# Optimization experiments

Measured on AMD Instinct MI355X. Metric: run time of the kernel, lower is better.

## Reference

```python
import jax, jax.numpy as jnp
import numpy as np

N, E, DIM, NF, ED = 15000, 30000, 64, 3, 1

def _gru_cell(x, h, w_ih, w_hh, b_ih, b_hh):
    gi = x @ w_ih.T + b_ih
    gh = h @ w_hh.T + b_hh
    ir, iz, i_n = jnp.split(gi, 3, axis=-1)
    hr, hz, hn = jnp.split(gh, 3, axis=-1)
    r = jax.nn.sigmoid(ir + hr)
    z = jax.nn.sigmoid(iz + hz)
    n = jnp.tanh(i_n + r * hn)
    return (1.0 - z) * n + z * h

def _lstm_cell(x, h, c, w_ih, w_hh, b_ih, b_hh):
    g = x @ w_ih.T + b_ih + h @ w_hh.T + b_hh
    i, f, gg, o = jnp.split(g, 4, axis=-1)
    c2 = jax.nn.sigmoid(f) * c + jax.nn.sigmoid(i) * jnp.tanh(gg)
    return jax.nn.sigmoid(o) * jnp.tanh(c2), c2

def setup_inputs():
    key = jax.random.key(0)
    ks = jax.random.split(key, 32)
    p = lambda k, shape: jax.random.normal(k, shape, jnp.float32) * 0.05
    return {
        "x": jax.random.normal(ks[0], (N, NF), jnp.float32),
        "edge_index": jax.random.randint(ks[1], (2, E), 0, N),
        "edge_attr": jax.random.uniform(ks[2], (E, ED), jnp.float32),
        "lin0_w": p(ks[3], (DIM, NF)), "lin0_b": p(ks[4], (DIM,)),
        "e1_w": p(ks[5], (DIM, ED)), "e1_b": p(ks[6], (DIM,)),
        "e2_w": p(ks[7], (DIM * DIM, DIM)), "e2_b": p(ks[8], (DIM * DIM,)),
        "root_w": p(ks[9], (DIM, DIM)), "conv_b": p(ks[10], (DIM,)),
        "gru_w_ih": p(ks[11], (3 * DIM, DIM)), "gru_w_hh": p(ks[12], (3 * DIM, DIM)),
        "gru_b_ih": p(ks[13], (3 * DIM,)), "gru_b_hh": p(ks[14], (3 * DIM,)),
        "s2s_w_ih": p(ks[15], (4 * DIM, 2 * DIM)), "s2s_w_hh": p(ks[16], (4 * DIM, DIM)),
        "s2s_b_ih": p(ks[17], (4 * DIM,)), "s2s_b_hh": p(ks[18], (4 * DIM,)),
        "mem_w_ih": p(ks[19], (4 * DIM, 2 * DIM)), "mem_w_hh": p(ks[20], (4 * DIM, DIM)),
        "mem_b_ih": p(ks[21], (4 * DIM,)), "mem_b_hh": p(ks[22], (4 * DIM,)),
        "lin1_w": p(ks[23], (DIM, DIM)), "lin1_b": p(ks[24], (DIM,)),
        "lin3_w": p(ks[25], (1, DIM)), "lin3_b": p(ks[26], (1,)),
    }

def reference(x, edge_index, edge_attr, lin0_w, lin0_b, e1_w, e1_b, e2_w, e2_b,
              root_w, conv_b, gru_w_ih, gru_w_hh, gru_b_ih, gru_b_hh,
              s2s_w_ih, s2s_w_hh, s2s_b_ih, s2s_b_hh,
              mem_w_ih, mem_w_hh, mem_b_ih, mem_b_hh,
              lin1_w, lin1_b, lin3_w, lin3_b):
    n = x.shape[0]
    src, dst = edge_index[0], edge_index[1]
    # per-edge weight matrices from the edge MLP: [E, DIM, DIM] (edge_attr is constant across the 6 conv steps)
    he = jax.nn.relu(edge_attr @ e1_w.T + e1_b)
    We = (he @ e2_w.T + e2_b).reshape(-1, DIM, DIM)
    deg = jax.ops.segment_sum(jnp.ones(src.shape[0], jnp.float32), dst, num_segments=n)
    denom = jnp.maximum(deg, 1.0)[:, None]
    out = jax.nn.relu(x @ lin0_w.T + lin0_b)   # [N, DIM]
    h = out                                    # GRU hidden init = lin0 output
    for _ in range(6):
        msg = jnp.einsum('ei,eio->eo', out[src], We)          # gather + per-edge matmul
        agg = jax.ops.segment_sum(msg, dst, num_segments=n) / denom  # mean aggr
        m = jax.nn.relu(agg + out @ root_w + conv_b)          # NNConv root + bias
        h = _gru_cell(m, h, gru_w_ih, gru_w_hh, gru_b_ih, gru_b_hh)
        out = h
    # Set2Set pooling over a single graph (data.batch is all zeros)
    q_star = jnp.zeros((1, 2 * DIM), x.dtype)
    hs = jnp.zeros((1, DIM), x.dtype)
    cs = jnp.zeros((1, DIM), x.dtype)
    for _ in range(6):
        hs, cs = _lstm_cell(q_star, hs, cs, s2s_w_ih, s2s_w_hh, s2s_b_ih, s2s_b_hh)
        e = out @ hs[0]                     # [N] attention logits
        a = jax.nn.softmax(e)
        r = (a[:, None] * out).sum(0, keepdims=True)  # [1, DIM]
        q_star = jnp.concatenate([hs, r], axis=-1)     # [1, 2*DIM]
    hx, cx = _lstm_cell(q_star, jnp.zeros((1, DIM), x.dtype), jnp.zeros((1, DIM), x.dtype),
                        mem_w_ih, mem_w_hh, mem_b_ih, mem_b_hh)
    o = jax.nn.relu(hx @ lin1_w.T + lin1_b)
    v = o @ lin3_w.T + lin3_b               # [1, 1]
    return v, hx, cx
```

## Files before the change

### kernel.cpp

```cpp
#include <hip/hip_runtime.h>
#include <math.h>

#define Nn 15000
#define NP 15040
#define Ee 30000
#define NB_E 118
#define EB 938

#define OFF_AGG   0
#define OFF_DEG   962560
#define ZERO_END  977560
#define OFF_OUT   977568
#define OFF_DINV  1940128
#define OFF_AT    1955136
#define OFF_BT    2221376
#define OFF_BP    2487616
#define OFF_U     2487680
#define OFF_V     2491840
#define OFF_MC    2496000
#define OFF_PE    2496016
#define OFF_BH    2526016
#define OFF_BC    2533696
#define OFF_SS    2541376
#define OFF_SD    2571376
#define OFF_SA    2601376
#define OFF_SP    2631376
#define OFF_PK    2661376
#define OFF_GMA   2690048
#define OFF_GSA   2690304
#define OFF_GRA   2690560
#define OFF_GMB   2706944
#define OFF_GSB   2707200
#define OFF_GRB   2707456
#define OFF_HS    2723840
#define OFF_CS    2723904
#define OFF_TSA   2723968
#define OFF_TSB   2740352
#define OFF_TMA   2756736
#define OFF_TMB   2773120
#define WS_FLOATS 2789504

__device__ __forceinline__ float sigf(float x) { return 1.0f / (1.0f + expf(-x)); }
__device__ __forceinline__ float bcast(float v, int l) {
    return __int_as_float(__builtin_amdgcn_readlane(__float_as_int(v), l));
}
__device__ __forceinline__ int bcasti(int v, int l) {
    return __builtin_amdgcn_readlane(v, l);
}

__global__ void k_lin0(const float* __restrict__ x, const float* __restrict__ w,
                       const float* __restrict__ b, float* __restrict__ out) {
    int idx = blockIdx.x * 256 + threadIdx.x;
    if (idx >= NP * 64) return;
    int n = idx >> 6, o = idx & 63;
    float v = 0.f;
    if (n < Nn)
        v = fmaxf(b[o] + x[n*3+0]*w[o*3+0] + x[n*3+1]*w[o*3+1] + x[n*3+2]*w[o*3+2], 0.f);
    out[idx] = v;
}

__global__ void k_patterns(const float* __restrict__ e1w, const float* __restrict__ e1b,
                           float* __restrict__ bp, float* __restrict__ u,
                           float* __restrict__ v, int* __restrict__ mc) {
    __shared__ float t[64]; __shared__ int valid[64]; __shared__ float sbp[65]; __shared__ int cnt;
    int k = threadIdx.x;
    float w1 = e1w[k], b1 = e1b[k];
    float tv = 0.f; int va = 0;
    if (w1 != 0.f) { tv = -b1 / w1; va = (tv > 0.f && tv < 1.f) ? 1 : 0; }
    t[k] = tv; valid[k] = va;
    __syncthreads();
    if (va) {
        int rank = 0;
        for (int kk = 0; kk < 64; ++kk)
            if (valid[kk] && (t[kk] < tv || (t[kk] == tv && kk < k))) rank++;
        sbp[rank] = tv;
    }
    if (k == 0) { int c = 0; for (int kk = 0; kk < 64; ++kk) c += valid[kk]; cnt = c; *mc = c; }
    __syncthreads();
    int m = cnt;
    if (k < m) bp[k] = sbp[k];
    for (int j = 0; j <= m; ++j) {
        float lo = (j == 0) ? 0.f : sbp[j-1];
        float hi = (j == m) ? 1.f : sbp[j];
        float c = 0.5f * (lo + hi);
        int msk = (c * w1 + b1) > 0.f;
        u[j*64 + k] = msk ? w1 : 0.f;
        v[j*64 + k] = msk ? b1 : 0.f;
    }
}

__global__ void k_AB2(const float* __restrict__ e2w, const float* __restrict__ e2b,
                      const float* __restrict__ u, const float* __restrict__ v,
                      const int* __restrict__ mc, float* __restrict__ At, float* __restrict__ Bt) {
    int j = blockIdx.x >> 4;
    if (j > *mc) return;
    int qc = blockIdx.x & 15;
    __shared__ float su[64], sv[64];
    if (threadIdx.x < 64) { su[threadIdx.x] = u[j*64+threadIdx.x]; sv[threadIdx.x] = v[j*64+threadIdx.x]; }
    __syncthreads();
    int q = qc*256 + threadIdx.x;
    int i = q >> 6, o = q & 63;
    const float* row = e2w + q*64;
    float a = 0.f, b = 0.f;
    #pragma unroll 8
    for (int k = 0; k < 64; ++k) { float w = row[k]; a = fmaf(su[k], w, a); b = fmaf(sv[k], w, b); }
    At[j*4096 + o*64 + i] = a;
    Bt[j*4096 + o*64 + i] = b + e2b[q];
}

__global__ void k_eprep2(const int* __restrict__ ei, const float* __restrict__ ea,
                         const float* __restrict__ bp, const int* __restrict__ mc,
                         float* __restrict__ deg, int* __restrict__ pe, int* __restrict__ bh) {
    __shared__ int lh[65];
    int tid = threadIdx.x;
    if (tid < 65) lh[tid] = 0;
    __syncthreads();
    int e = blockIdx.x * 256 + tid;
    if (e < Ee) {
        atomicAdd(&deg[ei[Ee + e]], 1.0f);
        float a = ea[e];
        int m = *mc, p = 0;
        for (int j = 0; j < m; ++j) p += (bp[j] <= a) ? 1 : 0;
        pe[e] = p;
        atomicAdd(&lh[p], 1);
    }
    __syncthreads();
    if (tid < 65) bh[blockIdx.x*65 + tid] = lh[tid];
}

__global__ void k_scan2(const float* __restrict__ deg, float* __restrict__ dinv,
                        const int* __restrict__ bh, int* __restrict__ bc) {
    int tid = threadIdx.x;
    if (blockIdx.x < 59) {
        int n = blockIdx.x * 256 + tid;
        if (n < Nn) dinv[n] = 1.0f / fmaxf(deg[n], 1.0f);
        return;
    }
    __shared__ int stot[65]; __shared__ int sbase[65];
    if (tid < 65) {
        int t = 0;
        for (int b = 0; b < NB_E; ++b) t += bh[b*65 + tid];
        stot[tid] = t;
    }
    __syncthreads();
    if (tid == 0) {
        int run = 0;
        for (int j = 0; j < 65; ++j) { sbase[j] = run; run += stot[j]; }
    }
    __syncthreads();
    if (tid < 65) {
        int run = sbase[tid];
        for (int b = 0; b < NB_E; ++b) { bc[b*65 + tid] = run; run += bh[b*65 + tid]; }
    }
}

__global__ void k_scatter2(const int* __restrict__ ei, const float* __restrict__ ea,
                           const int* __restrict__ pe, const int* __restrict__ bc,
                           int* __restrict__ sS, int* __restrict__ sD,
                           float* __restrict__ sA, int* __restrict__ sP) {
    __shared__ int cur[65];
    int tid = threadIdx.x;
    if (tid < 65) cur[tid] = bc[blockIdx.x*65 + tid];
    __syncthreads();
    int e = blockIdx.x * 256 + tid;
    if (e >= Ee) return;
    int p = pe[e];
    int pos = atomicAdd(&cur[p], 1);
    sS[pos] = ei[e]; sD[pos] = ei[Ee + e]; sA[pos] = ea[e]; sP[pos] = p;
}

__global__ void k_wt2(const float* __restrict__ rootw, const float* __restrict__ whh,
                      const float* __restrict__ wih, float* __restrict__ pk) {
    int idx = blockIdx.x * 256 + threadIdx.x;
    if (idx >= 7*4096) return;
    int g = idx >> 12;
    int t = idx & 4095;
    int q4 = t >> 2, k = t & 3;
    int lane = q4 & 63;
    int i4 = q4 >> 6;
    int i = i4*4 + k;
    float v;
    if (g == 0)      v = rootw[i*64 + lane];
    else if (g < 4)  v = whh[((g-1)*64 + lane)*64 + i];
    else             v = wih[((g-4)*64 + lane)*64 + i];
    pk[idx] = v;
}

__global__ void k_wt3(const float* __restrict__ swih, const float* __restrict__ swhh,
                      const float* __restrict__ mwih,
                      float* __restrict__ sa, float* __restrict__ sb,
                      float* __restrict__ ma, float* __restrict__ mb) {
    int idx = blockIdx.x * 256 + threadIdx.x;
    if (idx >= 4*16384) return;
    int t = idx >> 14, r = idx & 16383;
    int i = r >> 8, g = r & 255;
    if (t == 0)      sa[r] = swih[g*128 + i] + swhh[g*64 + i];
    else if (t == 1) sb[r] = swih[g*128 + 64 + i];
    else if (t == 2) ma[r] = mwih[g*128 + i];
    else             mb[r] = mwih[g*128 + 64 + i];
}

__global__ __launch_bounds__(256) void k_edge4(
        const int* __restrict__ sS, const int* __restrict__ sD,
        const float* __restrict__ sA, const int* __restrict__ sP,
        const float* __restrict__ out, const float* __restrict__ At,
        const float* __restrict__ Bt, const float* __restrict__ dinv,
        float* __restrict__ agg) {
    int tid = threadIdx.x, lane = tid & 63;
    int wid = (blockIdx.x * 256 + tid) >> 6;
    const int CH = 8;
    int e0 = wid * CH;
    if (e0 >= Ee) return;
    int e1 = e0 + CH; if (e1 > Ee) e1 = Ee;
    int cnt = e1 - e0;

    int eidx = e0 + lane;
    int msrc = 0, mdst = 0, mp = 0; float ma = 0.f, mdv = 0.f;
    if (lane < cnt) {
        msrc = sS[eidx]; mdst = sD[eidx]; ma = sA[eidx]; mp = sP[eidx];
        mdv = dinv[mdst];
    }

    float Ar[64], Br[64];
    int curp = -1;
    float hv_next = out[bcasti(msrc, 0)*64 + lane];
    for (int j = 0; j < cnt; ++j) {
        float hv = hv_next;
        if (j+1 < cnt) hv_next = out[bcasti(msrc, j+1)*64 + lane];
        int p = bcasti(mp, j);
        if (p != curp) {
            curp = p;
            const float4* Ap4 = (const float4*)(At + p*4096 + lane*64);
            const float4* Bp4 = (const float4*)(Bt + p*4096 + lane*64);
            #pragma unroll
            for (int q = 0; q < 16; ++q) {
                float4 av = Ap4[q], bv = Bp4[q];
                Ar[q*4+0]=av.x; Ar[q*4+1]=av.y; Ar[q*4+2]=av.z; Ar[q*4+3]=av.w;
                Br[q*4+0]=bv.x; Br[q*4+1]=bv.y; Br[q*4+2]=bv.z; Br[q*4+3]=bv.w;
            }
        }
        float a = bcast(ma, j);
        float acc0 = 0.f, acc1 = 0.f;
        #pragma unroll
        for (int i = 0; i < 64; i += 2) {
            float h0 = bcast(hv, i);
            float h1 = bcast(hv, i+1);
            acc0 = fmaf(h0, fmaf(a, Ar[i],   Br[i]),   acc0);
            acc1 = fmaf(h1, fmaf(a, Ar[i+1], Br[i+1]), acc1);
        }
        float acc = (acc0 + acc1) * bcast(mdv, j);
        atomicAdd(&agg[bcasti(mdst, j)*64 + lane], acc);
    }
}

__global__ __launch_bounds__(512, 2) void k_gru9(
        float* __restrict__ out, float* __restrict__ agg,
        const float* __restrict__ pk, const float* __restrict__ convb,
        const float* __restrict__ gbih, const float* __restrict__ gbhh) {
    __shared__ __align__(16) float wL[7*4096];
    int tid = threadIdx.x, lane = tid & 63, w = tid >> 6;
    {
        const float4* src = (const float4*)pk;
        float4* dst = (float4*)wL;
        #pragma unroll
        for (int i = 0; i < 14; ++i) dst[i*512 + tid] = src[i*512 + tid];
    }
    __syncthreads();
    const float4* wL4 = (const float4*)wL;
    int n0 = blockIdx.x*64 + w*8;

    float hv[8], mv[8], ghr[8], ghz[8], ghn[8];
    #pragma unroll
    for (int k = 0; k < 8; ++k) hv[k] = out[(n0+k)*64 + lane];

    float a0[8], a1[8], a2[8], a3[8];
    #pragma unroll
    for (int k = 0; k < 8; ++k) { a0[k]=0.f; a1[k]=0.f; a2[k]=0.f; a3[k]=0.f; }
    #pragma unroll 4
    for (int i4 = 0; i4 < 16; ++i4) {
        float4 w0 = wL4[(0*16+i4)*64 + lane];
        float4 w1 = wL4[(1*16+i4)*64 + lane];
        float4 w2 = wL4[(2*16+i4)*64 + lane];
        float4 w3 = wL4[(3*16+i4)*64 + lane];
        #pragma unroll
        for (int k = 0; k < 8; ++k) {
            float h;
            h = bcast(hv[k], i4*4+0);
            a0[k]=fmaf(h,w0.x,a0[k]); a1[k]=fmaf(h,w1.x,a1[k]);
            a2[k]=fmaf(h,w2.x,a2[k]); a3[k]=fmaf(h,w3.x,a3[k]);
            h = bcast(hv[k], i4*4+1);
            a0[k]=fmaf(h,w0.y,a0[k]); a1[k]=fmaf(h,w1.y,a1[k]);
            a2[k]=fmaf(h,w2.y,a2[k]); a3[k]=fmaf(h,w3.y,a3[k]);
            h = bcast(hv[k], i4*4+2);
            a0[k]=fmaf(h,w0.z,a0[k]); a1[k]=fmaf(h,w1.z,a1[k]);
            a2[k]=fmaf(h,w2.z,a2[k]); a3[k]=fmaf(h,w3.z,a3[k]);
            h = bcast(hv[k], i4*4+3);
            a0[k]=fmaf(h,w0.w,a0[k]); a1[k]=fmaf(h,w1.w,a1[k]);
            a2[k]=fmaf(h,w2.w,a2[k]); a3[k]=fmaf(h,w3.w,a3[k]);
        }
    }
    float cbv = convb[lane];
    #pragma unroll
    for (int k = 0; k < 8; ++k) {
        int gi = (n0+k)*64 + lane;
        float av = agg[gi]; agg[gi] = 0.f;
        mv[k] = fmaxf(a0[k] + av + cbv, 0.f);
        ghr[k] = a1[k]; ghz[k] = a2[k]; ghn[k] = a3[k];
    }

    #pragma unroll
    for (int k = 0; k < 8; ++k) { a0[k]=0.f; a1[k]=0.f; a2[k]=0.f; }
    #pragma unroll 4
    for (int i4 = 0; i4 < 16; ++i4) {
        float4 w4v = wL4[(4*16+i4)*64 + lane];
        float4 w5v = wL4[(5*16+i4)*64 + lane];
        float4 w6v = wL4[(6*16+i4)*64 + lane];
        #pragma unroll
        for (int k = 0; k < 8; ++k) {
            float h;
            h = bcast(mv[k], i4*4+0);
            a0[k]=fmaf(h,w4v.x,a0[k]); a1[k]=fmaf(h,w5v.x,a1[k]); a2[k]=fmaf(h,w6v.x,a2[k]);
            h = bcast(mv[k], i4*4+1);
            a0[k]=fmaf(h,w4v.y,a0[k]); a1[k]=fmaf(h,w5v.y,a1[k]); a2[k]=fmaf(h,w6v.y,a2[k]);
            h = bcast(mv[k], i4*4+2);
            a0[k]=fmaf(h,w4v.z,a0[k]); a1[k]=fmaf(h,w5v.z,a1[k]); a2[k]=fmaf(h,w6v.z,a2[k]);
            h = bcast(mv[k], i4*4+3);
            a0[k]=fmaf(h,w4v.w,a0[k]); a1[k]=fmaf(h,w5v.w,a1[k]); a2[k]=fmaf(h,w6v.w,a2[k]);
        }
    }

    float br  = gbih[lane]      + gbhh[lane];
    float bz  = gbih[64+lane]   + gbhh[64+lane];
    float bnI = gbih[128+lane];
    float bnH = gbhh[128+lane];
    #pragma unroll
    for (int k = 0; k < 8; ++k) {
        float r  = sigf(a0[k] + ghr[k] + br);
        float z  = sigf(a1[k] + ghz[k] + bz);
        float nn = tanhf(fmaf(r, ghn[k] + bnH, a2[k] + bnI));
        out[(n0+k)*64 + lane] = (1.f - z)*nn + z*hv[k];
    }
}

__global__ __launch_bounds__(512) void k_s2s(
        const float* __restrict__ tsa, const float* __restrict__ tsb,
        const float* __restrict__ bih, const float* __restrict__ bhh,
        float* __restrict__ hs, float* __restrict__ cs,
        const float* __restrict__ out,
        const float* __restrict__ gmax_rd, const float* __restrict__ gsum_rd,
        const float* __restrict__ gr_rd,
        float* __restrict__ gmax_wr, float* __restrict__ gsum_wr,
        float* __restrict__ gr_wr, int it) {
    __shared__ float red[512], shs[64], scs[64], srv[64], sg[256];
    __shared__ float sm_m[8], sm_z[8], sm_r[8][64];
    int tid = threadIdx.x, lane = tid & 63, w = tid >> 6;
    if (it == 0) {
        if (tid < 64) { shs[tid] = 0.f; scs[tid] = 0.f; srv[tid] = 0.f; }
    } else {
        float gm = (tid < 256) ? gmax_rd[tid] : -3.4e38f;
        red[tid] = gm; __syncthreads();
        for (int s = 256; s > 0; s >>= 1) { if (tid < s) red[tid] = fmaxf(red[tid], red[tid+s]); __syncthreads(); }
        float M = red[0]; __syncthreads();
        red[tid] = (tid < 256) ? gsum_rd[tid] * expf(gm - M) : 0.f; __syncthreads();
        for (int s = 256; s > 0; s >>= 1) { if (tid < s) red[tid] += red[tid+s]; __syncthreads(); }
        float Z = red[0]; __syncthreads();
        float racc = 0.f;
        for (int b = w; b < 256; b += 8) racc = fmaf(gr_rd[b*64 + lane], expf(gmax_rd[b] - M), racc);
        red[tid] = racc; __syncthreads();
        if (w == 0) {
            float s = 0.f;
            #pragma unroll
            for (int k = 0; k < 8; ++k) s += red[k*64 + lane];
            srv[lane] = s / Z;
        }
        if (tid < 64) { shs[tid] = hs[tid]; scs[tid] = cs[tid]; }
    }
    __syncthreads();
    if (tid < 256) {
        float g = bih[tid] + bhh[tid];
        #pragma unroll 8
        for (int i = 0; i < 64; ++i)
            g += shs[i]*tsa[i*256 + tid] + srv[i]*tsb[i*256 + tid];
        sg[tid] = g;
    }
    __syncthreads();
    if (tid < 64) {
        float ii = sigf(sg[tid]), ff = sigf(sg[64+tid]);
        float gg = tanhf(sg[128+tid]), oo = sigf(sg[192+tid]);
        float c2 = ff*scs[tid] + ii*gg;
        float hn = oo*tanhf(c2);
        shs[tid] = hn;
        if (blockIdx.x == 0) { hs[tid] = hn; cs[tid] = c2; }
    }
    __syncthreads();
    float hsv = shs[lane];
    float m = -3.4e38f, Z2 = 0.f, racc2 = 0.f;
    for (int n = blockIdx.x*8 + w; n < Nn; n += 2048) {
        float ov = out[n*64 + lane];
        float p = ov * hsv;
        #pragma unroll
        for (int off = 32; off > 0; off >>= 1) p += __shfl_xor(p, off, 64);
        float mn = fmaxf(m, p);
        float sc = expf(m - mn);
        float t  = expf(p - mn);
        Z2 = fmaf(Z2, sc, t);
        racc2 = fmaf(racc2, sc, t*ov);
        m = mn;
    }
    if (lane == 0) { sm_m[w] = m; sm_z[w] = Z2; }
    sm_r[w][lane] = racc2;
    __syncthreads();
    if (w == 0) {
        float M = sm_m[0];
        #pragma unroll
        for (int j = 1; j < 8; ++j) M = fmaxf(M, sm_m[j]);
        float Zb = 0.f, rb = 0.f;
        #pragma unroll
        for (int j = 0; j < 8; ++j) {
            float e = expf(sm_m[j] - M);
            Zb = fmaf(sm_z[j], e, Zb);
            rb = fmaf(sm_r[j][lane], e, rb);
        }
        gr_wr[blockIdx.x*64 + lane] = rb;
        if (lane == 0) { gmax_wr[blockIdx.x] = M; gsum_wr[blockIdx.x] = Zb; }
    }
}

__global__ __launch_bounds__(256) void k_final2(
        const float* __restrict__ tma, const float* __restrict__ tmb,
        const float* __restrict__ mbih, const float* __restrict__ mbhh,
        const float* __restrict__ hs,
        const float* __restrict__ gmax, const float* __restrict__ gsum,
        const float* __restrict__ gr,
        const float* __restrict__ l1w, const float* __restrict__ l1b,
        const float* __restrict__ l3w, const float* __restrict__ l3b,
        float* __restrict__ dout) {
    __shared__ float red[256], shs[64], srv[64], sg[256], shx[64], so[64];
    int tid = threadIdx.x, lane = tid & 63, w = tid >> 6;
    {
        float gm = gmax[tid];
        red[tid] = gm; __syncthreads();
        for (int s = 128; s > 0; s >>= 1) { if (tid < s) red[tid] = fmaxf(red[tid], red[tid+s]); __syncthreads(); }
        float M = red[0]; __syncthreads();
        red[tid] = gsum[tid] * expf(gm - M); __syncthreads();
        for (int s = 128; s > 0; s >>= 1) { if (tid < s) red[tid] += red[tid+s]; __syncthreads(); }
        float Z = red[0]; __syncthreads();
        float racc = 0.f;
        for (int b = w; b < 256; b += 4) racc = fmaf(gr[b*64 + lane], expf(gmax[b] - M), racc);
        red[tid] = racc; __syncthreads();
        if (w == 0) srv[lane] = (red[lane] + red[64+lane] + red[128+lane] + red[192+lane]) / Z;
        if (tid < 64) shs[tid] = hs[tid];
    }
    __syncthreads();
    {
        float g = mbih[tid] + mbhh[tid];
        #pragma unroll 8
        for (int i = 0; i < 64; ++i)
            g += shs[i]*tma[i*256 + tid] + srv[i]*tmb[i*256 + tid];
        sg[tid] = g;
    }
    __syncthreads();
    if (tid < 64) {
        float ii = sigf(sg[tid]);
        float gg = tanhf(sg[128+tid]);
        float oo = sigf(sg[192+tid]);
        float c2 = ii * gg;
        float hx = oo * tanhf(c2);
        shx[tid] = hx;
        dout[1 + tid] = hx;
        dout[65 + tid] = c2;
    }
    __syncthreads();
    if (tid < 64) {
        float a = l1b[tid];
        const float* wr = l1w + tid*64;
        #pragma unroll 8
        for (int i = 0; i < 64; ++i) a = fmaf(shx[i], wr[i], a);
        so[tid] = fmaxf(a, 0.f);
    }
    __syncthreads();
    if (tid == 0) {
        float v = l3b[0];
        for (int i = 0; i < 64; ++i) v = fmaf(so[i], l3w[i], v);
        dout[0] = v;
    }
}

extern "C" void kernel_launch(void* const* d_in, const int* in_sizes, int n_in,
                              void* d_out, int out_size, void* d_ws, size_t ws_size,
                              hipStream_t stream) {
    const float* x    = (const float*)d_in[0];
    const int*   ei   = (const int*)  d_in[1];
    const float* ea   = (const float*)d_in[2];
    const float* l0w  = (const float*)d_in[3];
    const float* l0b  = (const float*)d_in[4];
    const float* e1w  = (const float*)d_in[5];
    const float* e1b  = (const float*)d_in[6];
    const float* e2w  = (const float*)d_in[7];
    const float* e2b  = (const float*)d_in[8];
    const float* rootw= (const float*)d_in[9];
    const float* convb= (const float*)d_in[10];
    const float* gwih = (const float*)d_in[11];
    const float* gwhh = (const float*)d_in[12];
    const float* gbih = (const float*)d_in[13];
    const float* gbhh = (const float*)d_in[14];
    const float* swih = (const float*)d_in[15];
    const float* swhh = (const float*)d_in[16];
    const float* sbih = (const float*)d_in[17];
    const float* sbhh = (const float*)d_in[18];
    const float* mwih = (const float*)d_in[19];
    const float* mbih = (const float*)d_in[21];
    const float* mbhh = (const float*)d_in[22];
    const float* l1w  = (const float*)d_in[23];
    const float* l1b  = (const float*)d_in[24];
    const float* l3w  = (const float*)d_in[25];
    const float* l3b  = (const float*)d_in[26];

    float* ws   = (float*)d_ws;
    float* dout = (float*)d_out;
    if (ws_size < (size_t)WS_FLOATS * sizeof(float)) return;

    float* agg  = ws + OFF_AGG;
    float* deg  = ws + OFF_DEG;
    float* out  = ws + OFF_OUT;
    float* dinv = ws + OFF_DINV;
    float* At   = ws + OFF_AT;
    float* Bt   = ws + OFF_BT;
    float* bp   = ws + OFF_BP;
    float* ubuf = ws + OFF_U;
    float* vbuf = ws + OFF_V;
    int*   mc   = (int*)(ws + OFF_MC);
    int*   pe   = (int*)(ws + OFF_PE);
    int*   bh   = (int*)(ws + OFF_BH);
    int*   bc   = (int*)(ws + OFF_BC);
    int*   sS   = (int*)(ws + OFF_SS);
    int*   sD   = (int*)(ws + OFF_SD);
    float* sA   = ws + OFF_SA;
    int*   sP   = (int*)(ws + OFF_SP);
    float* pk   = ws + OFF_PK;
    float* gmA  = ws + OFF_GMA;
    float* gsA  = ws + OFF_GSA;
    float* grA  = ws + OFF_GRA;
    float* gmB  = ws + OFF_GMB;
    float* gsB  = ws + OFF_GSB;
    float* grB  = ws + OFF_GRB;
    float* hs   = ws + OFF_HS;
    float* cs   = ws + OFF_CS;
    float* tsa  = ws + OFF_TSA;
    float* tsb  = ws + OFF_TSB;
    float* tma  = ws + OFF_TMA;
    float* tmb  = ws + OFF_TMB;

    hipMemsetAsync(d_ws, 0, (size_t)ZERO_END * sizeof(float), stream);

    k_lin0    <<<(NP*64 + 255)/256, 256, 0, stream>>>(x, l0w, l0b, out);
    k_patterns<<<1, 64, 0, stream>>>(e1w, e1b, bp, ubuf, vbuf, mc);
    k_AB2     <<<65*16, 256, 0, stream>>>(e2w, e2b, ubuf, vbuf, mc, At, Bt);
    k_eprep2  <<<NB_E, 256, 0, stream>>>(ei, ea, bp, mc, deg, pe, bh);
    k_scan2   <<<60, 256, 0, stream>>>(deg, dinv, bh, bc);
    k_scatter2<<<NB_E, 256, 0, stream>>>(ei, ea, pe, bc, sS, sD, sA, sP);
    k_wt2     <<<(7*4096 + 255)/256, 256, 0, stream>>>(rootw, gwhh, gwih, pk);
    k_wt3     <<<(4*16384 + 255)/256, 256, 0, stream>>>(swih, swhh, mwih, tsa, tsb, tma, tmb);

    for (int s = 0; s < 6; ++s) {
        k_edge4<<<EB, 256, 0, stream>>>(sS, sD, sA, sP, out, At, Bt, dinv, agg);
        k_gru9 <<<NP/64, 512, 0, stream>>>(out, agg, pk, convb, gbih, gbhh);
    }

    for (int it = 0; it < 6; ++it) {
        float* gm_rd = (it & 1) ? gmA : gmB;
        float* gs_rd = (it & 1) ? gsA : gsB;
        float* gr_rd = (it & 1) ? grA : grB;
        float* gm_wr = (it & 1) ? gmB : gmA;
        float* gs_wr = (it & 1) ? gsB : gsA;
        float* gr_wr = (it & 1) ? grB : grA;
        k_s2s<<<256, 512, 0, stream>>>(tsa, tsb, sbih, sbhh, hs, cs, out,
                                       gm_rd, gs_rd, gr_rd, gm_wr, gs_wr, gr_wr, it);
    }

    k_final2<<<1, 256, 0, stream>>>(tma, tmb, mbih, mbhh, hs, gmB, gsB, grB,
                                    l1w, l1b, l3w, l3b, dout);
}
```

Measured before the change: 453.2 us.

## Fuse setup kernels and memset into block-dispatched launches, use wave-shuffle reductions

Merges lin0, pattern detection, the two weight-transpose kernels and the workspace memset into one block-indexed k_setup launch, and merges AB2 with edge prep into k_prep. This cuts the number of launches and the dependency bubbles between the many small setup kernels. The Set2Set and final kernels replace their shared-memory tree reductions with wave shuffle reductions, which removes many __syncthreads. The risk is in the block-range boundaries and the zero-fill size: they must match the workspace layout exactly.

```diff
diff --git a/kernel.cpp b/kernel.cpp
--- a/kernel.cpp
+++ b/kernel.cpp
@@ -40,6 +40,14 @@
 #define OFF_TMB   2773120
 #define WS_FLOATS 2789504
 
+#define SB_LIN0   3760
+#define SB_PAT    3760
+#define SB_WT2    3761
+#define SB_WT3    3873
+#define SB_ZERO   4129
+#define SB_TOTAL  5084
+#define ZERO_F4   244390
+
 __device__ __forceinline__ float sigf(float x) { return 1.0f / (1.0f + expf(-x)); }
 __device__ __forceinline__ float bcast(float v, int l) {
     return __int_as_float(__builtin_amdgcn_readlane(__float_as_int(v), l));
@@ -48,84 +56,127 @@
     return __builtin_amdgcn_readlane(v, l);
 }
 
-__global__ void k_lin0(const float* __restrict__ x, const float* __restrict__ w,
-                       const float* __restrict__ b, float* __restrict__ out) {
-    int idx = blockIdx.x * 256 + threadIdx.x;
-    if (idx >= NP * 64) return;
-    int n = idx >> 6, o = idx & 63;
-    float v = 0.f;
-    if (n < Nn)
-        v = fmaxf(b[o] + x[n*3+0]*w[o*3+0] + x[n*3+1]*w[o*3+1] + x[n*3+2]*w[o*3+2], 0.f);
-    out[idx] = v;
-}
-
-__global__ void k_patterns(const float* __restrict__ e1w, const float* __restrict__ e1b,
-                           float* __restrict__ bp, float* __restrict__ u,
-                           float* __restrict__ v, int* __restrict__ mc) {
-    __shared__ float t[64]; __shared__ int valid[64]; __shared__ float sbp[65]; __shared__ int cnt;
-    int k = threadIdx.x;
-    float w1 = e1w[k], b1 = e1b[k];
-    float tv = 0.f; int va = 0;
-    if (w1 != 0.f) { tv = -b1 / w1; va = (tv > 0.f && tv < 1.f) ? 1 : 0; }
-    t[k] = tv; valid[k] = va;
-    __syncthreads();
-    if (va) {
-        int rank = 0;
-        for (int kk = 0; kk < 64; ++kk)
-            if (valid[kk] && (t[kk] < tv || (t[kk] == tv && kk < k))) rank++;
-        sbp[rank] = tv;
-    }
-    if (k == 0) { int c = 0; for (int kk = 0; kk < 64; ++kk) c += valid[kk]; cnt = c; *mc = c; }
-    __syncthreads();
-    int m = cnt;
-    if (k < m) bp[k] = sbp[k];
-    for (int j = 0; j <= m; ++j) {
-        float lo = (j == 0) ? 0.f : sbp[j-1];
-        float hi = (j == m) ? 1.f : sbp[j];
-        float c = 0.5f * (lo + hi);
-        int msk = (c * w1 + b1) > 0.f;
-        u[j*64 + k] = msk ? w1 : 0.f;
-        v[j*64 + k] = msk ? b1 : 0.f;
-    }
-}
-
-__global__ void k_AB2(const float* __restrict__ e2w, const float* __restrict__ e2b,
-                      const float* __restrict__ u, const float* __restrict__ v,
-                      const int* __restrict__ mc, float* __restrict__ At, float* __restrict__ Bt) {
-    int j = blockIdx.x >> 4;
-    if (j > *mc) return;
-    int qc = blockIdx.x & 15;
-    __shared__ float su[64], sv[64];
-    if (threadIdx.x < 64) { su[threadIdx.x] = u[j*64+threadIdx.x]; sv[threadIdx.x] = v[j*64+threadIdx.x]; }
-    __syncthreads();
-    int q = qc*256 + threadIdx.x;
-    int i = q >> 6, o = q & 63;
-    const float* row = e2w + q*64;
-    float a = 0.f, b = 0.f;
-    #pragma unroll 8
-    for (int k = 0; k < 64; ++k) { float w = row[k]; a = fmaf(su[k], w, a); b = fmaf(sv[k], w, b); }
-    At[j*4096 + o*64 + i] = a;
-    Bt[j*4096 + o*64 + i] = b + e2b[q];
-}
-
-__global__ void k_eprep2(const int* __restrict__ ei, const float* __restrict__ ea,
-                         const float* __restrict__ bp, const int* __restrict__ mc,
-                         float* __restrict__ deg, int* __restrict__ pe, int* __restrict__ bh) {
-    __shared__ int lh[65];
-    int tid = threadIdx.x;
-    if (tid < 65) lh[tid] = 0;
-    __syncthreads();
-    int e = blockIdx.x * 256 + tid;
-    if (e < Ee) {
-        atomicAdd(&deg[ei[Ee + e]], 1.0f);
-        float a = ea[e];
-        int m = *mc, p = 0;
-        for (int j = 0; j < m; ++j) p += (bp[j] <= a) ? 1 : 0;
-        pe[e] = p;
-        atomicAdd(&lh[p], 1);
-    }
-    __syncthreads();
-    if (tid < 65) bh[blockIdx.x*65 + tid] = lh[tid];
+__global__ __launch_bounds__(256) void k_setup(
+        const float* __restrict__ x, const float* __restrict__ l0w,
+        const float* __restrict__ l0b, float* __restrict__ out,
+        const float* __restrict__ e1w, const float* __restrict__ e1b,
+        float* __restrict__ bp, float* __restrict__ u, float* __restrict__ v,
+        int* __restrict__ mc,
+        const float* __restrict__ rootw, const float* __restrict__ whh,
+        const float* __restrict__ wih, float* __restrict__ pk,
+        const float* __restrict__ swih, const float* __restrict__ swhh,
+        const float* __restrict__ mwih,
+        float* __restrict__ tsa, float* __restrict__ tsb,
+        float* __restrict__ tma, float* __restrict__ tmb,
+        float* __restrict__ zbase) {
+    int b = blockIdx.x, tid = threadIdx.x;
+    if (b < SB_LIN0) {
+        int idx = b*256 + tid;
+        int n = idx >> 6, o = idx & 63;
+        float vv = 0.f;
+        if (n < Nn)
+            vv = fmaxf(l0b[o] + x[n*3+0]*l0w[o*3+0] + x[n*3+1]*l0w[o*3+1]
+                       + x[n*3+2]*l0w[o*3+2], 0.f);
+        out[idx] = vv;
+    } else if (b == SB_PAT) {
+        __shared__ float t[64]; __shared__ int valid[64];
+        __shared__ float sbp[65]; __shared__ int cnt;
+        int k = tid;
+        float w1 = 0.f, b1 = 0.f, tv = 0.f; int va = 0;
+        if (k < 64) {
+            w1 = e1w[k]; b1 = e1b[k];
+            if (w1 != 0.f) { tv = -b1 / w1; va = (tv > 0.f && tv < 1.f) ? 1 : 0; }
+            t[k] = tv; valid[k] = va;
+        }
+        __syncthreads();
+        if (k < 64 && va) {
+            int rank = 0;
+            for (int kk = 0; kk < 64; ++kk)
+                if (valid[kk] && (t[kk] < tv || (t[kk] == tv && kk < k))) rank++;
+            sbp[rank] = tv;
+        }
+        if (k == 0) { int c = 0; for (int kk = 0; kk < 64; ++kk) c += valid[kk]; cnt = c; *mc = c; }
+        __syncthreads();
+        if (k < 64) {
+            int m = cnt;
+            if (k < m) bp[k] = sbp[k];
+            for (int j = 0; j <= m; ++j) {
+                float lo = (j == 0) ? 0.f : sbp[j-1];
+                float hi = (j == m) ? 1.f : sbp[j];
+                float c = 0.5f * (lo + hi);
+                int msk = (c * w1 + b1) > 0.f;
+                u[j*64 + k] = msk ? w1 : 0.f;
+                v[j*64 + k] = msk ? b1 : 0.f;
+            }
+        }
+    } else if (b < SB_WT3) {
+        int idx = (b - SB_WT2)*256 + tid;
+        int g = idx >> 12;
+        int t2 = idx & 4095;
+        int q4 = t2 >> 2, k = t2 & 3;
+        int lane = q4 & 63;
+        int i4 = q4 >> 6;
+        int i = i4*4 + k;
+        float vv;
+        if (g == 0)      vv = rootw[i*64 + lane];
+        else if (g < 4)  vv = whh[((g-1)*64 + lane)*64 + i];
+        else             vv = wih[((g-4)*64 + lane)*64 + i];
+        pk[idx] = vv;
+    } else if (b < SB_ZERO) {
+        int idx = (b - SB_WT3)*256 + tid;
+        int t2 = idx >> 14, r = idx & 16383;
+        int i = r >> 8, g = r & 255;
+        if (t2 == 0)      tsa[r] = swih[g*128 + i] + swhh[g*64 + i];
+        else if (t2 == 1) tsb[r] = swih[g*128 + 64 + i];
+        else if (t2 == 2) tma[r] = mwih[g*128 + i];
+        else              tmb[r] = mwih[g*128 + 64 + i];
+    } else {
+        int idx = (b - SB_ZERO)*256 + tid;
+        if (idx < ZERO_F4)
+            ((float4*)zbase)[idx] = make_float4(0.f, 0.f, 0.f, 0.f);
+    }
+}
+
+__global__ __launch_bounds__(256) void k_prep(
+        const float* __restrict__ e2w, const float* __restrict__ e2b,
+        const float* __restrict__ u, const float* __restrict__ v,
+        const int* __restrict__ mc, float* __restrict__ At, float* __restrict__ Bt,
+        const int* __restrict__ ei, const float* __restrict__ ea,
+        const float* __restrict__ bp, float* __restrict__ deg,
+        int* __restrict__ pe, int* __restrict__ bh) {
+    int b = blockIdx.x, tid = threadIdx.x;
+    if (b < 1040) {
+        int j = b >> 4;
+        if (j > *mc) return;
+        int qc = b & 15;
+        __shared__ float su[64], sv[64];
+        if (tid < 64) { su[tid] = u[j*64+tid]; sv[tid] = v[j*64+tid]; }
+        __syncthreads();
+        int q = qc*256 + tid;
+        int i = q >> 6, o = q & 63;
+        const float* row = e2w + q*64;
+        float a = 0.f, bb = 0.f;
+        #pragma unroll 8
+        for (int k = 0; k < 64; ++k) { float w = row[k]; a = fmaf(su[k], w, a); bb = fmaf(sv[k], w, bb); }
+        At[j*4096 + o*64 + i] = a;
+        Bt[j*4096 + o*64 + i] = bb + e2b[q];
+    } else {
+        int eb = b - 1040;
+        __shared__ int lh[65];
+        if (tid < 65) lh[tid] = 0;
+        __syncthreads();
+        int e = eb * 256 + tid;
+        if (e < Ee) {
+            atomicAdd(&deg[ei[Ee + e]], 1.0f);
+            float a = ea[e];
+            int m = *mc, p = 0;
+            for (int j = 0; j < m; ++j) p += (bp[j] <= a) ? 1 : 0;
+            pe[e] = p;
+            atomicAdd(&lh[p], 1);
+        }
+        __syncthreads();
+        if (tid < 65) bh[eb*65 + tid] = lh[tid];
+    }
 }
 
 __global__ void k_scan2(const float* __restrict__ deg, float* __restrict__ dinv,
@@ -167,37 +218,6 @@
     int p = pe[e];
     int pos = atomicAdd(&cur[p], 1);
     sS[pos] = ei[e]; sD[pos] = ei[Ee + e]; sA[pos] = ea[e]; sP[pos] = p;
-}
-
-__global__ void k_wt2(const float* __restrict__ rootw, const float* __restrict__ whh,
-                      const float* __restrict__ wih, float* __restrict__ pk) {
-    int idx = blockIdx.x * 256 + threadIdx.x;
-    if (idx >= 7*4096) return;
-    int g = idx >> 12;
-    int t = idx & 4095;
-    int q4 = t >> 2, k = t & 3;
-    int lane = q4 & 63;
-    int i4 = q4 >> 6;
-    int i = i4*4 + k;
-    float v;
-    if (g == 0)      v = rootw[i*64 + lane];
-    else if (g < 4)  v = whh[((g-1)*64 + lane)*64 + i];
-    else             v = wih[((g-4)*64 + lane)*64 + i];
-    pk[idx] = v;
-}
-
-__global__ void k_wt3(const float* __restrict__ swih, const float* __restrict__ swhh,
-                      const float* __restrict__ mwih,
-                      float* __restrict__ sa, float* __restrict__ sb,
-                      float* __restrict__ ma, float* __restrict__ mb) {
-    int idx = blockIdx.x * 256 + threadIdx.x;
-    if (idx >= 4*16384) return;
-    int t = idx >> 14, r = idx & 16383;
-    int i = r >> 8, g = r & 255;
-    if (t == 0)      sa[r] = swih[g*128 + i] + swhh[g*64 + i];
-    else if (t == 1) sb[r] = swih[g*128 + 64 + i];
-    else if (t == 2) ma[r] = mwih[g*128 + i];
-    else             mb[r] = mwih[g*128 + 64 + i];
 }
 
 __global__ __launch_bounds__(256) void k_edge4(
@@ -352,30 +372,40 @@
         float* __restrict__ gmax_wr, float* __restrict__ gsum_wr,
         float* __restrict__ gr_wr, int it) {
     __shared__ float red[512], shs[64], scs[64], srv[64], sg[256];
+    __shared__ float wred[8], zred[8];
     __shared__ float sm_m[8], sm_z[8], sm_r[8][64];
     int tid = threadIdx.x, lane = tid & 63, w = tid >> 6;
     if (it == 0) {
         if (tid < 64) { shs[tid] = 0.f; scs[tid] = 0.f; srv[tid] = 0.f; }
+        __syncthreads();
     } else {
         float gm = (tid < 256) ? gmax_rd[tid] : -3.4e38f;
-        red[tid] = gm; __syncthreads();
-        for (int s = 256; s > 0; s >>= 1) { if (tid < s) red[tid] = fmaxf(red[tid], red[tid+s]); __syncthreads(); }
-        float M = red[0]; __syncthreads();
-        red[tid] = (tid < 256) ? gsum_rd[tid] * expf(gm - M) : 0.f; __syncthreads();
-        for (int s = 256; s > 0; s >>= 1) { if (tid < s) red[tid] += red[tid+s]; __syncthreads(); }
-        float Z = red[0]; __syncthreads();
+        float wm = gm;
+        #pragma unroll
+        for (int off = 32; off > 0; off >>= 1) wm = fmaxf(wm, __shfl_xor(wm, off, 64));
+        if (lane == 0) wred[w] = wm;
+        __syncthreads();
+        float M = fmaxf(fmaxf(fmaxf(wred[0], wred[1]), fmaxf(wred[2], wred[3])),
+                        fmaxf(fmaxf(wred[4], wred[5]), fmaxf(wred[6], wred[7])));
+        float zt = (tid < 256) ? gsum_rd[tid] * expf(gm - M) : 0.f;
+        #pragma unroll
+        for (int off = 32; off > 0; off >>= 1) zt += __shfl_xor(zt, off, 64);
+        if (lane == 0) zred[w] = zt;
         float racc = 0.f;
-        for (int b = w; b < 256; b += 8) racc = fmaf(gr_rd[b*64 + lane], expf(gmax_rd[b] - M), racc);
-        red[tid] = racc; __syncthreads();
+        for (int b2 = w; b2 < 256; b2 += 8)
+            racc = fmaf(gr_rd[b2*64 + lane], expf(gmax_rd[b2] - M), racc);
+        red[tid] = racc;
+        if (tid < 64) { shs[tid] = hs[tid]; scs[tid] = cs[tid]; }
+        __syncthreads();
         if (w == 0) {
+            float Z = zred[0]+zred[1]+zred[2]+zred[3]+zred[4]+zred[5]+zred[6]+zred[7];
             float s = 0.f;
             #pragma unroll
             for (int k = 0; k < 8; ++k) s += red[k*64 + lane];
             srv[lane] = s / Z;
         }
-        if (tid < 64) { shs[tid] = hs[tid]; scs[tid] = cs[tid]; }
-    }
-    __syncthreads();
+        __syncthreads();
+    }
     if (tid < 256) {
         float g = bih[tid] + bhh[tid];
         #pragma unroll 8
@@ -436,20 +466,30 @@
         const float* __restrict__ l3w, const float* __restrict__ l3b,
         float* __restrict__ dout) {
     __shared__ float red[256], shs[64], srv[64], sg[256], shx[64], so[64];
+    __shared__ float wred[4], zred[4];
     int tid = threadIdx.x, lane = tid & 63, w = tid >> 6;
     {
         float gm = gmax[tid];
-        red[tid] = gm; __syncthreads();
-        for (int s = 128; s > 0; s >>= 1) { if (tid < s) red[tid] = fmaxf(red[tid], red[tid+s]); __syncthreads(); }
-        float M = red[0]; __syncthreads();
-        red[tid] = gsum[tid] * expf(gm - M); __syncthreads();
-        for (int s = 128; s > 0; s >>= 1) { if (tid < s) red[tid] += red[tid+s]; __syncthreads(); }
-        float Z = red[0]; __syncthreads();
+        float wm = gm;
+        #pragma unroll
+        for (int off = 32; off > 0; off >>= 1) wm = fmaxf(wm, __shfl_xor(wm, off, 64));
+        if (lane == 0) wred[w] = wm;
+        __syncthreads();
+        float M = fmaxf(fmaxf(wred[0], wred[1]), fmaxf(wred[2], wred[3]));
+        float zt = gsum[tid] * expf(gm - M);
+        #pragma unroll
+        for (int off = 32; off > 0; off >>= 1) zt += __shfl_xor(zt, off, 64);
+        if (lane == 0) zred[w] = zt;
         float racc = 0.f;
-        for (int b = w; b < 256; b += 4) racc = fmaf(gr[b*64 + lane], expf(gmax[b] - M), racc);
-        red[tid] = racc; __syncthreads();
-        if (w == 0) srv[lane] = (red[lane] + red[64+lane] + red[128+lane] + red[192+lane]) / Z;
+        for (int b2 = w; b2 < 256; b2 += 4)
+            racc = fmaf(gr[b2*64 + lane], expf(gmax[b2] - M), racc);
+        red[tid] = racc;
         if (tid < 64) shs[tid] = hs[tid];
+        __syncthreads();
+        if (w == 0) {
+            float Z = zred[0]+zred[1]+zred[2]+zred[3];
+            srv[lane] = (red[lane] + red[64+lane] + red[128+lane] + red[192+lane]) / Z;
+        }
     }
     __syncthreads();
     {
@@ -551,16 +591,14 @@
     float* tma  = ws + OFF_TMA;
     float* tmb  = ws + OFF_TMB;
 
-    hipMemsetAsync(d_ws, 0, (size_t)ZERO_END * sizeof(float), stream);
-
-    k_lin0    <<<(NP*64 + 255)/256, 256, 0, stream>>>(x, l0w, l0b, out);
-    k_patterns<<<1, 64, 0, stream>>>(e1w, e1b, bp, ubuf, vbuf, mc);
-    k_AB2     <<<65*16, 256, 0, stream>>>(e2w, e2b, ubuf, vbuf, mc, At, Bt);
-    k_eprep2  <<<NB_E, 256, 0, stream>>>(ei, ea, bp, mc, deg, pe, bh);
+    k_setup   <<<SB_TOTAL, 256, 0, stream>>>(x, l0w, l0b, out, e1w, e1b, bp, ubuf,
+                                             vbuf, mc, rootw, gwhh, gwih, pk,
+                                             swih, swhh, mwih, tsa, tsb, tma, tmb,
+                                             ws + OFF_AGG);
+    k_prep    <<<1040 + NB_E, 256, 0, stream>>>(e2w, e2b, ubuf, vbuf, mc, At, Bt,
+                                                ei, ea, bp, deg, pe, bh);
     k_scan2   <<<60, 256, 0, stream>>>(deg, dinv, bh, bc);
     k_scatter2<<<NB_E, 256, 0, stream>>>(ei, ea, pe, bc, sS, sD, sA, sP);
-    k_wt2     <<<(7*4096 + 255)/256, 256, 0, stream>>>(rootw, gwhh, gwih, pk);
-    k_wt3     <<<(4*16384 + 255)/256, 256, 0, stream>>>(swih, swhh, mwih, tsa, tsb, tma, tmb);
 
     for (int s = 0; s < 6; ++s) {
         k_edge4<<<EB, 256, 0, stream>>>(sS, sD, sA, sP, out, At, Bt, dinv, agg);
```

After: 436.2 us. 3.7% less time.
